# Performance work log

Hardware: AMD Instinct MI355X
Metric: run time of the kernel (lower is better)

The kernel has to match this reference:

```python
import jax, jax.numpy as jnp
import numpy as np

EPS = 1e-6

def _rmsnorm(h, w):
    # RMSNorm: h * rsqrt(mean(h^2)) * w
    var = jnp.mean(jnp.square(h), axis=-1, keepdims=True)
    return h * jax.lax.rsqrt(var + EPS) * w

def setup_inputs() -> dict:
    key = jax.random.key(0)
    ks = jax.random.split(key, 9)
    B, N, L, D, C = 2, 4096, 256, 2048, 6
    s = 0.02
    return {
        "x": jax.random.normal(ks[0], (B, N, D), jnp.float32),
        "text_emb": jax.random.normal(ks[1], (B, L, D), jnp.float32),
        "Wc": jax.random.normal(ks[2], (C, D), jnp.float32) * s,
        "Wq": jax.random.normal(ks[3], (D, D), jnp.float32) * s,
        "Wk": jax.random.normal(ks[4], (D, D), jnp.float32) * s,
        "Wv": jax.random.normal(ks[5], (D, D), jnp.float32) * s,
        "Wo": jax.random.normal(ks[6], (D, D), jnp.float32) * s,
        "blend_weights": jnp.ones((C,), jnp.float32) / C + jax.random.normal(ks[7], (C,), jnp.float32) * 0.1,
        "surreal_gate": jnp.zeros((1,), jnp.float32),
        "norm_weight": jnp.ones((D,), jnp.float32),
        "is_surreal": 1,
    }

def reference(x, text_emb, Wc, Wq, Wk, Wv, Wo, blend_weights, surreal_gate, norm_weight, is_surreal):
    B, N, D = x.shape
    # soft concept clustering over text tokens
    cluster_logits = jnp.einsum('bld,cd->blc', text_emb, Wc)
    cluster_weights = jax.nn.softmax(cluster_logits, axis=-1)
    concept_reps = jnp.einsum('blc,bld->bcd', cluster_weights, text_emb)  # (B,C,D)
    # SDPA with a single key/value per concept: softmax over 1 key == 1, so the
    # attention output is exactly v broadcast over the N query tokens (q and k
    # cancel out of the math entirely; their grads are zero).
    v = jnp.einsum('bcd,ed->bce', concept_reps, Wv)  # (B,C,D) == per-concept output
    blend = jax.nn.softmax(blend_weights, axis=0)
    fused_bd = jnp.einsum('c,bcd->bd', blend, v)  # (B,D)
    if is_surreal:
        gate = jax.nn.sigmoid(surreal_gate)  # (1,)
        contradiction = jnp.var(v, axis=1, ddof=1)  # torch .var() is unbiased
        fused_bd = fused_bd + gate * contradiction * 0.3
    # broadcast to (B,N,D) as the torch module materializes, then norm + out_proj
    fused = jnp.broadcast_to(fused_bd[:, None, :], (B, N, D))
    out = jnp.einsum('bnd,ed->bne', _rmsnorm(fused, norm_weight), Wo)
    return x + out
```

## Files before the change

### kernel.cpp

```cpp
#include <hip/hip_runtime.h>
#include <hip/hip_bf16.h>

#define BB 2
#define NN 4096
#define LL 256
#define DD 2048
#define CC 6
#define EPSF 1e-6f

__device__ __forceinline__ float dot4(float4 a, float4 b) {
    return a.x * b.x + a.y * b.y + a.z * b.z + a.w * b.w;
}

__global__ __launch_bounds__(256) void k_cluster(const float* __restrict__ te,
                                                 const float* __restrict__ Wc,
                                                 float* __restrict__ cw) {
    const int row = blockIdx.x;
    const float4* t4 = (const float4*)(te + (size_t)row * DD);
    float p[CC];
#pragma unroll
    for (int c = 0; c < CC; ++c) p[c] = 0.f;
#pragma unroll
    for (int it = 0; it < DD / 4 / 256; ++it) {
        const int i = it * 256 + threadIdx.x;
        const float4 xv = t4[i];
#pragma unroll
        for (int c = 0; c < CC; ++c) {
            const float4 wv = ((const float4*)(Wc + (size_t)c * DD))[i];
            p[c] += dot4(xv, wv);
        }
    }
#pragma unroll
    for (int c = 0; c < CC; ++c)
        for (int off = 32; off; off >>= 1) p[c] += __shfl_down(p[c], off);
    __shared__ float sred[4][CC];
    const int lane = threadIdx.x & 63, wid = threadIdx.x >> 6;
    if (lane == 0) {
#pragma unroll
        for (int c = 0; c < CC; ++c) sred[wid][c] = p[c];
    }
    __syncthreads();
    if (threadIdx.x == 0) {
        float lg[CC], m = -1e30f;
#pragma unroll
        for (int c = 0; c < CC; ++c) {
            lg[c] = sred[0][c] + sred[1][c] + sred[2][c] + sred[3][c];
            m = fmaxf(m, lg[c]);
        }
        float s = 0.f;
#pragma unroll
        for (int c = 0; c < CC; ++c) { lg[c] = __expf(lg[c] - m); s += lg[c]; }
        float inv = 1.f / s;
#pragma unroll
        for (int c = 0; c < CC; ++c) cw[row * CC + c] = lg[c] * inv;
    }
}

__global__ __launch_bounds__(256) void k_creps(const float* __restrict__ te,
                                               const float* __restrict__ cw,
                                               float* __restrict__ cr) {
    const int b = blockIdx.x >> 5;
    const int d0 = (blockIdx.x & 31) * 64;
    __shared__ float scw[LL * CC];
    for (int i = threadIdx.x; i < LL * CC; i += 256) scw[i] = cw[b * LL * CC + i];
    __syncthreads();
    const int dl = threadIdx.x & 63;
    const int lc = threadIdx.x >> 6;
    float acc[CC];
#pragma unroll
    for (int c = 0; c < CC; ++c) acc[c] = 0.f;
    const float* tb = te + ((size_t)b * LL + lc * 64) * DD + d0 + dl;
    for (int l = 0; l < 64; ++l) {
        const float xv = tb[(size_t)l * DD];
        const int gl = lc * 64 + l;
#pragma unroll
        for (int c = 0; c < CC; ++c) acc[c] = fmaf(scw[gl * CC + c], xv, acc[c]);
    }
    __shared__ float sacc[4][64][CC];
#pragma unroll
    for (int c = 0; c < CC; ++c) sacc[lc][dl][c] = acc[c];
    __syncthreads();
    if (threadIdx.x < 64) {
#pragma unroll
        for (int c = 0; c < CC; ++c) {
            const float s = sacc[0][threadIdx.x][c] + sacc[1][threadIdx.x][c] +
                            sacc[2][threadIdx.x][c] + sacc[3][threadIdx.x][c];
            cr[((size_t)b * CC + c) * DD + d0 + threadIdx.x] = s;
        }
    }
}

__global__ __launch_bounds__(256) void k_vfuse(const float* __restrict__ cr,
                                               const float* __restrict__ Wv,
                                               const float* __restrict__ blendw,
                                               const float* __restrict__ sgate,
                                               const int* __restrict__ issur,
                                               float* __restrict__ fused) {
    const int e = blockIdx.x * 4 + (threadIdx.x >> 6);
    const int lane = threadIdx.x & 63;
    float acc[BB][CC];
#pragma unroll
    for (int b = 0; b < BB; ++b)
#pragma unroll
        for (int c = 0; c < CC; ++c) acc[b][c] = 0.f;
#pragma unroll
    for (int it = 0; it < DD / 256; ++it) {
        const int d = it * 256 + lane * 4;
        const float4 wv = *(const float4*)(Wv + (size_t)e * DD + d);
#pragma unroll
        for (int b = 0; b < BB; ++b)
#pragma unroll
            for (int c = 0; c < CC; ++c) {
                const float4 cv = *(const float4*)(cr + ((size_t)b * CC + c) * DD + d);
                acc[b][c] += dot4(cv, wv);
            }
    }
#pragma unroll
    for (int b = 0; b < BB; ++b)
#pragma unroll
        for (int c = 0; c < CC; ++c)
            for (int off = 32; off; off >>= 1) acc[b][c] += __shfl_down(acc[b][c], off);
    if (lane == 0) {
        float bw[CC], m = -1e30f;
#pragma unroll
        for (int c = 0; c < CC; ++c) { bw[c] = blendw[c]; m = fmaxf(m, bw[c]); }
        float s = 0.f;
#pragma unroll
        for (int c = 0; c < CC; ++c) { bw[c] = __expf(bw[c] - m); s += bw[c]; }
        const float inv = 1.f / s;
#pragma unroll
        for (int c = 0; c < CC; ++c) bw[c] *= inv;
        const float gate = 1.f / (1.f + __expf(-sgate[0]));
        const int sur = issur[0];
#pragma unroll
        for (int b = 0; b < BB; ++b) {
            float f = 0.f, mean = 0.f;
#pragma unroll
            for (int c = 0; c < CC; ++c) {
                f = fmaf(bw[c], acc[b][c], f);
                mean += acc[b][c];
            }
            mean *= (1.f / CC);
            float var = 0.f;
#pragma unroll
            for (int c = 0; c < CC; ++c) {
                const float dv = acc[b][c] - mean;
                var = fmaf(dv, dv, var);
            }
            var *= (1.f / (CC - 1));
            if (sur) f = fmaf(gate * var, 0.3f, f);
            fused[b * DD + e] = f;
        }
    }
}

__global__ __launch_bounds__(256) void k_rmsout(const float* __restrict__ fused,
                                                const float* __restrict__ nw,
                                                const float* __restrict__ Wo,
                                                float* __restrict__ o) {
    const int lane = threadIdx.x & 63, wid = threadIdx.x >> 6;
    float ss[BB];
#pragma unroll
    for (int b = 0; b < BB; ++b) ss[b] = 0.f;
#pragma unroll
    for (int k = 0; k < DD / 256; ++k) {
        const int d = k * 256 + threadIdx.x;
#pragma unroll
        for (int b = 0; b < BB; ++b) {
            const float v = fused[b * DD + d];
            ss[b] = fmaf(v, v, ss[b]);
        }
    }
#pragma unroll
    for (int b = 0; b < BB; ++b)
        for (int off = 32; off; off >>= 1) ss[b] += __shfl_down(ss[b], off);
    __shared__ float sred[4][BB];
    __shared__ float sscale[BB];
    if (lane == 0) {
#pragma unroll
        for (int b = 0; b < BB; ++b) sred[wid][b] = ss[b];
    }
    __syncthreads();
    if (threadIdx.x == 0) {
#pragma unroll
        for (int b = 0; b < BB; ++b) {
            const float tot = sred[0][b] + sred[1][b] + sred[2][b] + sred[3][b];
            sscale[b] = rsqrtf(tot * (1.f / DD) + EPSF);
        }
    }
    __syncthreads();
    const int e = blockIdx.x * 4 + wid;
    float acc[BB];
#pragma unroll
    for (int b = 0; b < BB; ++b) acc[b] = 0.f;
#pragma unroll
    for (int it = 0; it < DD / 256; ++it) {
        const int d = it * 256 + lane * 4;
        const float4 wv = *(const float4*)(Wo + (size_t)e * DD + d);
        const float4 nv = *(const float4*)(nw + d);
        float4 t;
        t.x = wv.x * nv.x; t.y = wv.y * nv.y; t.z = wv.z * nv.z; t.w = wv.w * nv.w;
#pragma unroll
        for (int b = 0; b < BB; ++b) {
            const float4 fv = *(const float4*)(fused + (size_t)b * DD + d);
            acc[b] += dot4(fv, t);
        }
    }
#pragma unroll
    for (int b = 0; b < BB; ++b) {
        for (int off = 32; off; off >>= 1) acc[b] += __shfl_down(acc[b], off);
        if (lane == 0) o[b * DD + e] = acc[b] * sscale[b];
    }
}

__global__ __launch_bounds__(256) void k_add(const float* __restrict__ x,
                                             const float* __restrict__ o,
                                             float* __restrict__ out) {
    const size_t total4 = (size_t)BB * NN * DD / 4;
    const float4* x4 = (const float4*)x;
    const float4* o4 = (const float4*)o;
    float4* out4 = (float4*)out;
    for (size_t f = (size_t)blockIdx.x * 256 + threadIdx.x; f < total4;
         f += (size_t)gridDim.x * 256) {
        const int e4 = (int)(f & (DD / 4 - 1));
        const int b = (int)(f >> 21);
        const float4 xv = x4[f];
        const float4 ov = o4[b * (DD / 4) + e4];
        float4 r;
        r.x = xv.x + ov.x; r.y = xv.y + ov.y;
        r.z = xv.z + ov.z; r.w = xv.w + ov.w;
        out4[f] = r;
    }
}

extern "C" void kernel_launch(void* const* d_in, const int* in_sizes, int n_in,
                              void* d_out, int out_size, void* d_ws, size_t ws_size,
                              hipStream_t stream) {
    const float* x  = (const float*)d_in[0];
    const float* te = (const float*)d_in[1];
    const float* Wc = (const float*)d_in[2];
    const float* Wv = (const float*)d_in[5];
    const float* Wo = (const float*)d_in[6];
    const float* bw = (const float*)d_in[7];
    const float* sg = (const float*)d_in[8];
    const float* nw = (const float*)d_in[9];
    const int* isur = (const int*)d_in[10];
    float* out = (float*)d_out;

    float* ws     = (float*)d_ws;
    float* cw     = ws;
    float* cr     = ws + 4096;
    float* fused  = ws + 4096 + 24576;
    float* o      = fused + 4096;

    hipLaunchKernelGGL(k_cluster, dim3(BB * LL), dim3(256), 0, stream, te, Wc, cw);
    hipLaunchKernelGGL(k_creps,   dim3(BB * 32), dim3(256), 0, stream, te, cw, cr);
    hipLaunchKernelGGL(k_vfuse,   dim3(DD / 4), dim3(256), 0, stream, cr, Wv, bw, sg, isur, fused);
    hipLaunchKernelGGL(k_rmsout,  dim3(DD / 4), dim3(256), 0, stream, fused, nw, Wo, o);
    hipLaunchKernelGGL(k_add,     dim3(2048), dim3(256), 0, stream, x, o, out);
}
```

Measured before the change: 52.22 us.

## Prefetch x and Wo into cache with extra blocks in earlier small kernels

Adds extra blocks to k_cluster and k_creps that load the two halves of x (64 MB) with no use except an asm keep, and extra blocks to k_vfuse that load Wo, so the data is warm in the MI355X last-level cache (Infinity Cache) when k_add and k_rmsout run. The goal is to overlap the main HBM streaming with the latency-bound early kernels. k_vfuse also computes two output rows per wave to reuse the cr loads, and k_add uses a fixed unrolled loop. The risk is that x (64 MB) may not stay resident in cache, so the prefetch would only add traffic.

```diff
diff --git a/kernel.cpp b/kernel.cpp
--- a/kernel.cpp
+++ b/kernel.cpp
@@ -12,35 +12,45 @@
     return a.x * b.x + a.y * b.y + a.z * b.z + a.w * b.w;
 }
 
+__device__ __forceinline__ void keep4(float4 v) {
+    asm volatile("" :: "v"(v.x), "v"(v.y), "v"(v.z), "v"(v.w));
+}
+
 __global__ __launch_bounds__(256) void k_cluster(const float* __restrict__ te,
                                                  const float* __restrict__ Wc,
-                                                 float* __restrict__ cw) {
+                                                 float* __restrict__ cw,
+                                                 const float4* __restrict__ x4) {
+    const int tid = threadIdx.x;
+    if (blockIdx.x >= 512) {
+        size_t i = (size_t)(blockIdx.x - 512) * 256 + tid;
+#pragma unroll
+        for (int k = 0; k < 16; ++k, i += 512 * 256) keep4(x4[i]);
+        return;
+    }
     const int row = blockIdx.x;
     const float4* t4 = (const float4*)(te + (size_t)row * DD);
     float p[CC];
 #pragma unroll
     for (int c = 0; c < CC; ++c) p[c] = 0.f;
 #pragma unroll
-    for (int it = 0; it < DD / 4 / 256; ++it) {
-        const int i = it * 256 + threadIdx.x;
+    for (int it = 0; it < 2; ++it) {
+        const int i = it * 256 + tid;
         const float4 xv = t4[i];
 #pragma unroll
-        for (int c = 0; c < CC; ++c) {
-            const float4 wv = ((const float4*)(Wc + (size_t)c * DD))[i];
-            p[c] += dot4(xv, wv);
-        }
+        for (int c = 0; c < CC; ++c)
+            p[c] += dot4(xv, ((const float4*)(Wc + (size_t)c * DD))[i]);
     }
 #pragma unroll
     for (int c = 0; c < CC; ++c)
         for (int off = 32; off; off >>= 1) p[c] += __shfl_down(p[c], off);
     __shared__ float sred[4][CC];
-    const int lane = threadIdx.x & 63, wid = threadIdx.x >> 6;
+    const int lane = tid & 63, wid = tid >> 6;
     if (lane == 0) {
 #pragma unroll
         for (int c = 0; c < CC; ++c) sred[wid][c] = p[c];
     }
     __syncthreads();
-    if (threadIdx.x == 0) {
+    if (tid == 0) {
         float lg[CC], m = -1e30f;
 #pragma unroll
         for (int c = 0; c < CC; ++c) {
@@ -50,7 +60,7 @@
         float s = 0.f;
 #pragma unroll
         for (int c = 0; c < CC; ++c) { lg[c] = __expf(lg[c] - m); s += lg[c]; }
-        float inv = 1.f / s;
+        const float inv = 1.f / s;
 #pragma unroll
         for (int c = 0; c < CC; ++c) cw[row * CC + c] = lg[c] * inv;
     }
@@ -58,34 +68,42 @@
 
 __global__ __launch_bounds__(256) void k_creps(const float* __restrict__ te,
                                                const float* __restrict__ cw,
-                                               float* __restrict__ cr) {
+                                               float* __restrict__ cr,
+                                               const float4* __restrict__ x4) {
+    const int tid = threadIdx.x;
+    if (blockIdx.x >= 64) {
+        const size_t HALF4 = (size_t)BB * NN * DD / 8;
+        size_t i = HALF4 + (size_t)(blockIdx.x - 64) * 256 + tid;
+#pragma unroll
+        for (int k = 0; k < 16; ++k, i += 512 * 256) keep4(x4[i]);
+        return;
+    }
     const int b = blockIdx.x >> 5;
     const int d0 = (blockIdx.x & 31) * 64;
+    const int lane = tid & 63, wid = tid >> 6;
     __shared__ float scw[LL * CC];
-    for (int i = threadIdx.x; i < LL * CC; i += 256) scw[i] = cw[b * LL * CC + i];
-    __syncthreads();
-    const int dl = threadIdx.x & 63;
-    const int lc = threadIdx.x >> 6;
+    __shared__ float sacc[4][64][CC];
+    for (int i = tid; i < LL * CC; i += 256) scw[i] = cw[b * LL * CC + i];
+    __syncthreads();
     float acc[CC];
 #pragma unroll
     for (int c = 0; c < CC; ++c) acc[c] = 0.f;
-    const float* tb = te + ((size_t)b * LL + lc * 64) * DD + d0 + dl;
+    const float* tb = te + ((size_t)b * LL + wid * 64) * DD + d0 + lane;
     for (int l = 0; l < 64; ++l) {
         const float xv = tb[(size_t)l * DD];
-        const int gl = lc * 64 + l;
+        const int gl = wid * 64 + l;
 #pragma unroll
         for (int c = 0; c < CC; ++c) acc[c] = fmaf(scw[gl * CC + c], xv, acc[c]);
     }
-    __shared__ float sacc[4][64][CC];
-#pragma unroll
-    for (int c = 0; c < CC; ++c) sacc[lc][dl][c] = acc[c];
-    __syncthreads();
-    if (threadIdx.x < 64) {
+#pragma unroll
+    for (int c = 0; c < CC; ++c) sacc[wid][lane][c] = acc[c];
+    __syncthreads();
+    if (tid < 64) {
 #pragma unroll
         for (int c = 0; c < CC; ++c) {
-            const float s = sacc[0][threadIdx.x][c] + sacc[1][threadIdx.x][c] +
-                            sacc[2][threadIdx.x][c] + sacc[3][threadIdx.x][c];
-            cr[((size_t)b * CC + c) * DD + d0 + threadIdx.x] = s;
+            const float s = sacc[0][tid][c] + sacc[1][tid][c] +
+                            sacc[2][tid][c] + sacc[3][tid][c];
+            cr[((size_t)b * CC + c) * DD + d0 + tid] = s;
         }
     }
 }
@@ -95,31 +113,46 @@
                                                const float* __restrict__ blendw,
                                                const float* __restrict__ sgate,
                                                const int* __restrict__ issur,
-                                               float* __restrict__ fused) {
-    const int e = blockIdx.x * 4 + (threadIdx.x >> 6);
-    const int lane = threadIdx.x & 63;
-    float acc[BB][CC];
+                                               float* __restrict__ fused,
+                                               const float4* __restrict__ Wo4) {
+    const int tid = threadIdx.x;
+    if (blockIdx.x >= 256) {
+        size_t i = (size_t)(blockIdx.x - 256) * 256 + tid;
+#pragma unroll
+        for (int k = 0; k < 16; ++k, i += 256 * 256) keep4(Wo4[i]);
+        return;
+    }
+    const int lane = tid & 63, wid = tid >> 6;
+    const int e0 = blockIdx.x * 8 + wid * 2;
+    float acc[BB][2][CC];
 #pragma unroll
     for (int b = 0; b < BB; ++b)
 #pragma unroll
-        for (int c = 0; c < CC; ++c) acc[b][c] = 0.f;
-#pragma unroll
-    for (int it = 0; it < DD / 256; ++it) {
+        for (int j = 0; j < 2; ++j)
+#pragma unroll
+            for (int c = 0; c < CC; ++c) acc[b][j][c] = 0.f;
+#pragma unroll
+    for (int it = 0; it < 8; ++it) {
         const int d = it * 256 + lane * 4;
-        const float4 wv = *(const float4*)(Wv + (size_t)e * DD + d);
+        const float4 w0 = *(const float4*)(Wv + (size_t)e0 * DD + d);
+        const float4 w1 = *(const float4*)(Wv + (size_t)(e0 + 1) * DD + d);
 #pragma unroll
         for (int b = 0; b < BB; ++b)
 #pragma unroll
             for (int c = 0; c < CC; ++c) {
                 const float4 cv = *(const float4*)(cr + ((size_t)b * CC + c) * DD + d);
-                acc[b][c] += dot4(cv, wv);
+                acc[b][0][c] += dot4(cv, w0);
+                acc[b][1][c] += dot4(cv, w1);
             }
     }
 #pragma unroll
     for (int b = 0; b < BB; ++b)
 #pragma unroll
-        for (int c = 0; c < CC; ++c)
-            for (int off = 32; off; off >>= 1) acc[b][c] += __shfl_down(acc[b][c], off);
+        for (int j = 0; j < 2; ++j)
+#pragma unroll
+            for (int c = 0; c < CC; ++c)
+                for (int off = 32; off; off >>= 1)
+                    acc[b][j][c] += __shfl_down(acc[b][j][c], off);
     if (lane == 0) {
         float bw[CC], m = -1e30f;
 #pragma unroll
@@ -133,24 +166,26 @@
         const float gate = 1.f / (1.f + __expf(-sgate[0]));
         const int sur = issur[0];
 #pragma unroll
-        for (int b = 0; b < BB; ++b) {
-            float f = 0.f, mean = 0.f;
-#pragma unroll
-            for (int c = 0; c < CC; ++c) {
-                f = fmaf(bw[c], acc[b][c], f);
-                mean += acc[b][c];
+        for (int b = 0; b < BB; ++b)
+#pragma unroll
+            for (int j = 0; j < 2; ++j) {
+                float f = 0.f, mean = 0.f;
+#pragma unroll
+                for (int c = 0; c < CC; ++c) {
+                    f = fmaf(bw[c], acc[b][j][c], f);
+                    mean += acc[b][j][c];
+                }
+                mean *= (1.f / CC);
+                float var = 0.f;
+#pragma unroll
+                for (int c = 0; c < CC; ++c) {
+                    const float dv = acc[b][j][c] - mean;
+                    var = fmaf(dv, dv, var);
+                }
+                var *= (1.f / (CC - 1));
+                if (sur) f = fmaf(gate * var, 0.3f, f);
+                fused[b * DD + e0 + j] = f;
             }
-            mean *= (1.f / CC);
-            float var = 0.f;
-#pragma unroll
-            for (int c = 0; c < CC; ++c) {
-                const float dv = acc[b][c] - mean;
-                var = fmaf(dv, dv, var);
-            }
-            var *= (1.f / (CC - 1));
-            if (sur) f = fmaf(gate * var, 0.3f, f);
-            fused[b * DD + e] = f;
-        }
     }
 }
 
@@ -158,13 +193,14 @@
                                                 const float* __restrict__ nw,
                                                 const float* __restrict__ Wo,
                                                 float* __restrict__ o) {
-    const int lane = threadIdx.x & 63, wid = threadIdx.x >> 6;
+    const int tid = threadIdx.x;
+    const int lane = tid & 63, wid = tid >> 6;
     float ss[BB];
 #pragma unroll
     for (int b = 0; b < BB; ++b) ss[b] = 0.f;
 #pragma unroll
     for (int k = 0; k < DD / 256; ++k) {
-        const int d = k * 256 + threadIdx.x;
+        const int d = k * 256 + tid;
 #pragma unroll
         for (int b = 0; b < BB; ++b) {
             const float v = fused[b * DD + d];
@@ -181,7 +217,7 @@
         for (int b = 0; b < BB; ++b) sred[wid][b] = ss[b];
     }
     __syncthreads();
-    if (threadIdx.x == 0) {
+    if (tid == 0) {
 #pragma unroll
         for (int b = 0; b < BB; ++b) {
             const float tot = sred[0][b] + sred[1][b] + sred[2][b] + sred[3][b];
@@ -216,12 +252,12 @@
 __global__ __launch_bounds__(256) void k_add(const float* __restrict__ x,
                                              const float* __restrict__ o,
                                              float* __restrict__ out) {
-    const size_t total4 = (size_t)BB * NN * DD / 4;
     const float4* x4 = (const float4*)x;
     const float4* o4 = (const float4*)o;
     float4* out4 = (float4*)out;
-    for (size_t f = (size_t)blockIdx.x * 256 + threadIdx.x; f < total4;
-         f += (size_t)gridDim.x * 256) {
+    size_t f = (size_t)blockIdx.x * 256 + threadIdx.x;
+#pragma unroll
+    for (int k = 0; k < 8; ++k, f += (size_t)2048 * 256) {
         const int e4 = (int)(f & (DD / 4 - 1));
         const int b = (int)(f >> 21);
         const float4 xv = x4[f];
@@ -250,12 +286,16 @@
     float* ws     = (float*)d_ws;
     float* cw     = ws;
     float* cr     = ws + 4096;
-    float* fused  = ws + 4096 + 24576;
-    float* o      = fused + 4096;
-
-    hipLaunchKernelGGL(k_cluster, dim3(BB * LL), dim3(256), 0, stream, te, Wc, cw);
-    hipLaunchKernelGGL(k_creps,   dim3(BB * 32), dim3(256), 0, stream, te, cw, cr);
-    hipLaunchKernelGGL(k_vfuse,   dim3(DD / 4), dim3(256), 0, stream, cr, Wv, bw, sg, isur, fused);
-    hipLaunchKernelGGL(k_rmsout,  dim3(DD / 4), dim3(256), 0, stream, fused, nw, Wo, o);
+    float* fusedv = ws + 4096 + 24576;
+    float* o      = fusedv + 4096;
+
+    hipLaunchKernelGGL(k_cluster, dim3(1024), dim3(256), 0, stream,
+                       te, Wc, cw, (const float4*)x);
+    hipLaunchKernelGGL(k_creps,   dim3(576),  dim3(256), 0, stream,
+                       te, cw, cr, (const float4*)x);
+    hipLaunchKernelGGL(k_vfuse,   dim3(512),  dim3(256), 0, stream,
+                       cr, Wv, bw, sg, isur, fusedv, (const float4*)Wo);
+    hipLaunchKernelGGL(k_rmsout,  dim3(DD / 4), dim3(256), 0, stream,
+                       fusedv, nw, Wo, o);
     hipLaunchKernelGGL(k_add,     dim3(2048), dim3(256), 0, stream, x, o, out);
 }
```

New measurement: 58.06 us. 11.2% more time.
